# Kernel optimization log

Hardware: AMD Instinct MI355X
Metric: run time of the kernel (lower is better)

The kernel has to match this reference:

```python
import jax, jax.numpy as jnp
import numpy as np

N = 20000      # nodes per type
E = 320000     # edges per relation
F = 512        # raw feature dim
H = 4          # attention heads
C = 128        # hidden_channels per head
B = 64         # batch_size (num graphs)
HH = H * C
INNER = 64
NEG_SLOPE = 0.2


def _gatv2(x_src, x_dst, ei, Wl, Wr, att, b):
    """PyG GATv2Conv (concat=True, add_self_loops=True, neg_slope=0.2).
    x_src:[Ns,Fin] x_dst:[Nd,Fin'] ei:[2,E] Wl,Wr:[Fin,H*C] att:[H,C] b:[H*C].
    Returns [Nd, H*C]. Self-loop edges appended (inputs assumed loop-free)."""
    n_dst = x_dst.shape[0]
    loop = jnp.arange(min(x_src.shape[0], n_dst), dtype=ei.dtype)
    src = jnp.concatenate([ei[0], loop])
    dst = jnp.concatenate([ei[1], loop])
    xl = (x_src @ Wl).reshape(-1, H, C)   # source-side transform
    xr = (x_dst @ Wr).reshape(-1, H, C)   # target-side transform
    e = jax.nn.leaky_relu(xl[src] + xr[dst], NEG_SLOPE)   # [E',H,C]
    logit = jnp.einsum('ehc,hc->eh', e, att)               # [E',H]
    m = jax.ops.segment_max(logit, dst, num_segments=n_dst)
    m = jnp.where(jnp.isfinite(m), m, 0.0)
    p = jnp.exp(logit - m[dst])
    s = jax.ops.segment_sum(p, dst, num_segments=n_dst)
    alpha = p / jnp.maximum(s[dst], 1e-16)                 # per-dst softmax
    out = jax.ops.segment_sum(alpha[:, :, None] * xl[src], dst, num_segments=n_dst)
    return out.reshape(n_dst, HH) + b


def _layer(x_i, x_j, ei_ii, ei_jj, ei_ij, ei_ji, Wl, Wr, att, b):
    # relation order: 0:(x_i->x_i) 1:(x_j->x_j) 2:(x_i->x_j) 3:(x_j->x_i); HeteroConv aggr='sum'
    oi = _gatv2(x_i, x_i, ei_ii, Wl[0], Wr[0], att[0], b[0]) \
       + _gatv2(x_j, x_i, ei_ji, Wl[3], Wr[3], att[3], b[3])
    oj = _gatv2(x_j, x_j, ei_jj, Wl[1], Wr[1], att[1], b[1]) \
       + _gatv2(x_i, x_j, ei_ij, Wl[2], Wr[2], att[2], b[2])
    # head-sum + tanh: x.view(-1, heads, hidden).sum(1).tanh()
    oi = jnp.tanh(oi.reshape(-1, H, C).sum(axis=1))
    oj = jnp.tanh(oj.reshape(-1, H, C).sum(axis=1))
    return oi, oj


def setup_inputs() -> dict:
    key = jax.random.key(0)
    ks = jax.random.split(key, 24)
    inp = {
        'x_i': jax.random.normal(ks[0], (N, F), jnp.float32),
        'x_j': jax.random.normal(ks[1], (N, F), jnp.float32),
        'ei_ii': jax.random.randint(ks[2], (2, E), 0, N, jnp.int32),
        'ei_jj': jax.random.randint(ks[3], (2, E), 0, N, jnp.int32),
        'ei_ij': jax.random.randint(ks[4], (2, E), 0, N, jnp.int32),
        'ei_ji': jax.random.randint(ks[5], (2, E), 0, N, jnp.int32),
        'batch_i': jnp.sort(jax.random.randint(ks[6], (N,), 0, B, jnp.int32)),
        'batch_j': jnp.sort(jax.random.randint(ks[7], (N,), 0, B, jnp.int32)),
        'Wl0': jax.random.normal(ks[8], (4, F, HH), jnp.float32) / np.sqrt(F),
        'Wr0': jax.random.normal(ks[9], (4, F, HH), jnp.float32) / np.sqrt(F),
        'att0': jax.random.normal(ks[10], (4, H, C), jnp.float32) / np.sqrt(C),
        'b0': jnp.zeros((4, HH), jnp.float32),
        'Wl1': jax.random.normal(ks[11], (4, C, HH), jnp.float32) / np.sqrt(C),
        'Wr1': jax.random.normal(ks[12], (4, C, HH), jnp.float32) / np.sqrt(C),
        'att1': jax.random.normal(ks[13], (4, H, C), jnp.float32) / np.sqrt(C),
        'b1': jnp.zeros((4, HH), jnp.float32),
        'W_out': jax.random.normal(ks[14], (C, 1), jnp.float32) / np.sqrt(C),
        'b_out': jnp.zeros((1,), jnp.float32),
        'W_i': jax.random.normal(ks[15], (C, INNER), jnp.float32) / np.sqrt(C),
        'b_i': jnp.zeros((INNER,), jnp.float32),
        'W_j': jax.random.normal(ks[16], (C, INNER), jnp.float32) / np.sqrt(C),
        'b_j': jnp.zeros((INNER,), jnp.float32),
    }
    return inp


def reference(x_i, x_j, ei_ii, ei_jj, ei_ij, ei_ji, batch_i, batch_j,
              Wl0, Wr0, att0, b0, Wl1, Wr1, att1, b1,
              W_out, b_out, W_i, b_i, W_j, b_j):
    x_i, x_j = _layer(x_i, x_j, ei_ii, ei_jj, ei_ij, ei_ji, Wl0, Wr0, att0, b0)
    x_i, x_j = _layer(x_i, x_j, ei_ii, ei_jj, ei_ij, ei_ji, Wl1, Wr1, att1, b1)
    # global_add_pool per graph, then unsqueeze(1) + tanh
    p_i = jnp.tanh(jax.ops.segment_sum(x_i, batch_i, num_segments=B))[:, None, :]  # [B,1,C]
    p_j = jnp.tanh(jax.ops.segment_sum(x_j, batch_j, num_segments=B))[:, None, :]
    y_i = p_i @ W_i + b_i   # [B,1,INNER]
    y_j = p_j @ W_j + b_j
    x = (p_i + p_j)[:, 0, :]            # cat along dim=1 then sum(dim=1)
    logits = jax.nn.sigmoid(x @ W_out + b_out)   # [B,1]
    return (logits, y_i, y_j)
```

## Files before the change

### kernel.cpp

```cpp
#include <hip/hip_runtime.h>

#define NN      20000
#define EE      320000
#define ETOT    340000
#define FD      512
#define HH_     4
#define CD      128
#define HHD     512
#define BG      64
#define INNERD  64

typedef __attribute__((ext_vector_type(8))) short bf16x8;
typedef __attribute__((ext_vector_type(4))) float f32x4;

__device__ __forceinline__ float bf2f(unsigned v) { return __uint_as_float(v << 16); }
__device__ __forceinline__ unsigned short f2bf(float f) {
    unsigned u = __float_as_uint(f);
    unsigned r = 0x7fffu + ((u >> 16) & 1u);
    return (unsigned short)((u + r) >> 16);
}
__device__ __forceinline__ void load8bf(const unsigned short* p, float* f) {
    uint4 u = *reinterpret_cast<const uint4*>(p);
    f[0] = bf2f(u.x & 0xffffu); f[1] = bf2f(u.x >> 16);
    f[2] = bf2f(u.y & 0xffffu); f[3] = bf2f(u.y >> 16);
    f[4] = bf2f(u.z & 0xffffu); f[5] = bf2f(u.z >> 16);
    f[6] = bf2f(u.w & 0xffffu); f[7] = bf2f(u.w >> 16);
}
__device__ __forceinline__ void split_f32(float x, unsigned short& hi, unsigned short& lo) {
    unsigned u = __float_as_uint(x);
    hi = (unsigned short)(u >> 16);
    float r = x - bf2f(hi);
    lo = (unsigned short)(__float_as_uint(r) >> 16);
}
template <typename TA>
__device__ __forceinline__ void splitA(const TA* p, size_t i, unsigned short& hi, unsigned short& lo);
template <>
__device__ __forceinline__ void splitA<float>(const float* p, size_t i, unsigned short& hi, unsigned short& lo) {
    split_f32(p[i], hi, lo);
}
template <>
__device__ __forceinline__ void splitA<unsigned short>(const unsigned short* p, size_t i, unsigned short& hi, unsigned short& lo) {
    hi = p[i]; lo = 0;
}

__global__ __launch_bounds__(256) void csr_hist(const int* __restrict__ ei, int* __restrict__ cnt) {
    int e = blockIdx.x * blockDim.x + threadIdx.x;
    if (e < EE) atomicAdd(&cnt[ei[EE + e]], 1);
}

__global__ __launch_bounds__(1024) void csr_scan(const int* __restrict__ cnt,
                                                 int* __restrict__ rowptr,
                                                 int* __restrict__ cursor) {
    __shared__ int part[1024];
    int t = threadIdx.x;
    int base = t * 20;
    int s = 0;
    #pragma unroll
    for (int i = 0; i < 20; ++i) { int n = base + i; if (n < NN) s += cnt[n] + 1; }
    part[t] = s;
    __syncthreads();
    for (int off = 1; off < 1024; off <<= 1) {
        int v = (t >= off) ? part[t - off] : 0;
        __syncthreads();
        part[t] += v;
        __syncthreads();
    }
    int run = (t > 0) ? part[t - 1] : 0;
    #pragma unroll
    for (int i = 0; i < 20; ++i) {
        int n = base + i;
        if (n < NN) { rowptr[n] = run; cursor[n] = run; run += cnt[n] + 1; }
    }
    if (t == 1023) rowptr[NN] = run;
}

__global__ __launch_bounds__(256) void csr_scatter16(const int* __restrict__ ei,
                                                     int* __restrict__ cursor,
                                                     unsigned short* __restrict__ srcs) {
    int idx = blockIdx.x * blockDim.x + threadIdx.x;
    if (idx >= ETOT) return;
    int src, dst;
    if (idx < EE) { src = ei[idx]; dst = ei[EE + idx]; }
    else          { src = dst = idx - EE; }
    int pos = atomicAdd(&cursor[dst], 1);
    srcs[pos] = (unsigned short)src;
}

__global__ __launch_bounds__(256) void wsplit_t(const float* __restrict__ W,
                                                unsigned short* __restrict__ Whi,
                                                unsigned short* __restrict__ Wlo,
                                                int K)
{
    __shared__ float tile[64][65];
    const int nt = 512 / 64;
    const int kt = K / 64;
    int bid = blockIdx.x;
    int in = bid % nt; int ik = (bid / nt) % kt; int r = bid / (nt * kt);
    int t = threadIdx.x;
    const float* Wr_ = W + (size_t)r * K * 512;
    #pragma unroll
    for (int rep = 0; rep < 16; ++rep) {
        int idx = rep * 256 + t;
        int kk = idx >> 6, nn = idx & 63;
        tile[kk][nn] = Wr_[(size_t)(ik * 64 + kk) * 512 + in * 64 + nn];
    }
    __syncthreads();
    #pragma unroll
    for (int rep = 0; rep < 16; ++rep) {
        int idx = rep * 256 + t;
        int nn = idx >> 6, kk = idx & 63;
        unsigned short h, l; split_f32(tile[kk][nn], h, l);
        int n = in * 64 + nn;
        int k = ik * 64 + kk;
        size_t o = (size_t)r * 512 * K + ((size_t)(k >> 5) * 512 + n) * 32 + (k & 31);
        Whi[o] = h; Wlo[o] = l;
    }
}

template <typename TA, bool A_EXACT>
__device__ __forceinline__ void gemm_body(
    const TA* __restrict__ A, const unsigned short* __restrict__ Bhg,
    const unsigned short* __restrict__ Blg, unsigned short* __restrict__ C,
    int bx, int by, int M, int K, int N)
{
    __shared__ unsigned short Ah[128][40];
    __shared__ unsigned short Al[A_EXACT ? 1 : 128][40];

    const int tid = threadIdx.x;
    const int wave = tid >> 6, lane = tid & 63;
    const int quad = lane >> 4, lrow = lane & 15;
    const int wr = (wave >> 1) * 64, wc = (wave & 1) * 64;
    const int tileM = by * 128, tileN = bx * 128;

    const int srow = tid >> 1;
    const int sks  = (tid & 1) * 16;
    const int sgm  = tileM + srow;

    const size_t bfrag = ((size_t)(tileN + wc + lrow) << 5) + quad * 8;
    const size_t kblk  = (size_t)N << 5;

    f32x4 acc[4][4] = {};

    for (int k0 = 0; k0 < K; k0 += 32) {
        if constexpr (!A_EXACT) {
            bf16x8 ph[2] = {{}, {}}, pl[2] = {{}, {}};
            if (sgm < M) {
                const float* Ap = (const float*)A + (size_t)sgm * K + k0 + sks;
                #pragma unroll
                for (int s = 0; s < 2; ++s) {
                    float4 f0 = reinterpret_cast<const float4*>(Ap)[2 * s];
                    float4 f1 = reinterpret_cast<const float4*>(Ap)[2 * s + 1];
                    float xv[8] = {f0.x, f0.y, f0.z, f0.w, f1.x, f1.y, f1.z, f1.w};
                    #pragma unroll
                    for (int pp = 0; pp < 4; ++pp) {
                        unsigned u0 = __float_as_uint(xv[2 * pp]);
                        unsigned u1 = __float_as_uint(xv[2 * pp + 1]);
                        reinterpret_cast<unsigned*>(&ph[s])[pp] =
                            __builtin_amdgcn_perm(u1, u0, 0x07060302u);
                        float r0 = xv[2 * pp]     - __uint_as_float(u0 & 0xffff0000u);
                        float r1 = xv[2 * pp + 1] - __uint_as_float(u1 & 0xffff0000u);
                        reinterpret_cast<unsigned*>(&pl[s])[pp] =
                            __builtin_amdgcn_perm(__float_as_uint(r1), __float_as_uint(r0), 0x07060302u);
                    }
                }
            }
            *reinterpret_cast<bf16x8*>(&Ah[srow][sks])     = ph[0];
            *reinterpret_cast<bf16x8*>(&Ah[srow][sks + 8]) = ph[1];
            *reinterpret_cast<bf16x8*>(&Al[srow][sks])     = pl[0];
            *reinterpret_cast<bf16x8*>(&Al[srow][sks + 8]) = pl[1];
        } else {
            bf16x8 v0 = {}, v1 = {};
            if (sgm < M) {
                const unsigned short* Ap = (const unsigned short*)A + (size_t)sgm * K + k0 + sks;
                v0 = reinterpret_cast<const bf16x8*>(Ap)[0];
                v1 = reinterpret_cast<const bf16x8*>(Ap)[1];
            }
            *reinterpret_cast<bf16x8*>(&Ah[srow][sks])     = v0;
            *reinterpret_cast<bf16x8*>(&Ah[srow][sks + 8]) = v1;
        }
        bf16x8 bh[4], bl[4];
        {
            const unsigned short* Bb = Bhg + (size_t)(k0 >> 5) * kblk + bfrag;
            const unsigned short* Bc = Blg + (size_t)(k0 >> 5) * kblk + bfrag;
            #pragma unroll
            for (int ni = 0; ni < 4; ++ni) {
                bh[ni] = *reinterpret_cast<const bf16x8*>(Bb + ((size_t)ni << 9));
                bl[ni] = *reinterpret_cast<const bf16x8*>(Bc + ((size_t)ni << 9));
            }
        }
        __syncthreads();
        bf16x8 ah[4], al[4];
        #pragma unroll
        for (int mi = 0; mi < 4; ++mi) {
            ah[mi] = *reinterpret_cast<const bf16x8*>(&Ah[wr + mi * 16 + lrow][quad * 8]);
            if constexpr (!A_EXACT)
                al[mi] = *reinterpret_cast<const bf16x8*>(&Al[wr + mi * 16 + lrow][quad * 8]);
        }
        #pragma unroll
        for (int mi = 0; mi < 4; ++mi)
            #pragma unroll
            for (int ni = 0; ni < 4; ++ni) {
                acc[mi][ni] = __builtin_amdgcn_mfma_f32_16x16x32_bf16(
                    ah[mi], bh[ni], acc[mi][ni], 0, 0, 0);
                acc[mi][ni] = __builtin_amdgcn_mfma_f32_16x16x32_bf16(
                    ah[mi], bl[ni], acc[mi][ni], 0, 0, 0);
                if constexpr (!A_EXACT)
                    acc[mi][ni] = __builtin_amdgcn_mfma_f32_16x16x32_bf16(
                        al[mi], bh[ni], acc[mi][ni], 0, 0, 0);
            }
        __syncthreads();
    }
    #pragma unroll
    for (int mi = 0; mi < 4; ++mi) {
        #pragma unroll
        for (int ni = 0; ni < 4; ++ni) {
            int gcol = tileN + wc + ni * 16 + lrow;
            #pragma unroll
            for (int r = 0; r < 4; ++r) {
                int grow = tileM + wr + mi * 16 + quad * 4 + r;
                if (grow < M)
                    C[(size_t)grow * N + gcol] = f2bf(acc[mi][ni][r]);
            }
        }
    }
}

template <typename TA, bool A_EXACT>
__global__ __launch_bounds__(256, 3) void gemm_mfma_t(
    const TA* __restrict__ A0, const TA* __restrict__ A1,
    const unsigned short* __restrict__ B0h, const unsigned short* __restrict__ B0l,
    const unsigned short* __restrict__ B1h, const unsigned short* __restrict__ B1l,
    unsigned short* __restrict__ C0, unsigned short* __restrict__ C1,
    int M, int K, int N)
{
    const int gx = gridDim.x, gy = gridDim.y;
    const int nwg = gx * gy * (int)gridDim.z;
    int b = ((int)blockIdx.z * gy + blockIdx.y) * gx + blockIdx.x;
    int xcd = b & 7, q8 = nwg >> 3, r8 = nwg & 7;
    int work = (xcd < r8 ? xcd * (q8 + 1) : r8 * (q8 + 1) + (xcd - r8) * q8) + (b >> 3);
    int bx = work % gx; int t2 = work / gx; int by = t2 % gy; int bz = t2 / gy;

    const TA* A = bz ? A1 : A0;
    const unsigned short* Bhg = bz ? B1h : B0h;
    const unsigned short* Blg = bz ? B1l : B0l;
    unsigned short* C = bz ? C1 : C0;
    gemm_body<TA, A_EXACT>(A, Bhg, Blg, C, bx, by, M, K, N);
}

template <typename TA, bool A_EXACT>
__global__ __launch_bounds__(256, 3) void gemm_mfma_t4(
    const TA* __restrict__ A0, const TA* __restrict__ A1,
    const TA* __restrict__ A2, const TA* __restrict__ A3,
    const unsigned short* __restrict__ B0h, const unsigned short* __restrict__ B0l,
    const unsigned short* __restrict__ B1h, const unsigned short* __restrict__ B1l,
    const unsigned short* __restrict__ B2h, const unsigned short* __restrict__ B2l,
    const unsigned short* __restrict__ B3h, const unsigned short* __restrict__ B3l,
    unsigned short* __restrict__ C0, unsigned short* __restrict__ C1,
    unsigned short* __restrict__ C2, unsigned short* __restrict__ C3,
    int M, int K, int N)
{
    const int gx = gridDim.x, gy = gridDim.y;
    const int nwg = gx * gy * (int)gridDim.z;
    int b = ((int)blockIdx.z * gy + blockIdx.y) * gx + blockIdx.x;
    int xcd = b & 7, q8 = nwg >> 3, r8 = nwg & 7;
    int work = (xcd < r8 ? xcd * (q8 + 1) : r8 * (q8 + 1) + (xcd - r8) * q8) + (b >> 3);
    int bx = work % gx; int t2 = work / gx; int by = t2 % gy; int bz = t2 / gy;

    const TA* A = bz == 0 ? A0 : bz == 1 ? A1 : bz == 2 ? A2 : A3;
    const unsigned short* Bhg = bz == 0 ? B0h : bz == 1 ? B1h : bz == 2 ? B2h : B3h;
    const unsigned short* Blg = bz == 0 ? B0l : bz == 1 ? B1l : bz == 2 ? B2l : B3l;
    unsigned short* C = bz == 0 ? C0 : bz == 1 ? C1 : bz == 2 ? C2 : C3;
    gemm_body<TA, A_EXACT>(A, Bhg, Blg, C, bx, by, M, K, N);
}

template <typename TA, bool A_EXACT>
__global__ __launch_bounds__(256) void gemm_mfma(
    const TA* __restrict__ A0, const TA* __restrict__ A1,
    const float* __restrict__ B0, const float* __restrict__ B1, int ldb,
    unsigned short* __restrict__ C0, unsigned short* __restrict__ C1,
    int M, int K, int N)
{
    const TA* A = blockIdx.z ? A1 : A0;
    const float* B = blockIdx.z ? B1 : B0;
    unsigned short* C = blockIdx.z ? C1 : C0;

    __shared__ unsigned short Ah[64][40];
    __shared__ unsigned short Al[64][40];
    __shared__ unsigned short Bh[64][40];
    __shared__ unsigned short Bl[64][40];
    const int tid = threadIdx.x;
    const int wave = tid >> 6, lane = tid & 63;
    const int quad = lane >> 4, lrow = lane & 15;
    const int tileM = blockIdx.y * 64, tileN = blockIdx.x * 64;
    const int wm = (wave >> 1) * 32, wn = (wave & 1) * 32;

    f32x4 acc[2][2] = {};

    const int am = tid >> 2;
    const int aks = (tid & 3) * 8;
    const int bn = tid & 63;
    const int bk0 = (tid >> 6) * 8;

    for (int k0 = 0; k0 < K; k0 += 32) {
        {
            int gm = tileM + am;
            bf16x8 ph = {}, pl = {};
            if (gm < M) {
                #pragma unroll
                for (int j = 0; j < 8; ++j) {
                    unsigned short h, l;
                    splitA(A, (size_t)gm * K + k0 + aks + j, h, l);
                    ph[j] = (short)h; pl[j] = (short)l;
                }
            }
            *reinterpret_cast<bf16x8*>(&Ah[am][aks]) = ph;
            if (!A_EXACT) *reinterpret_cast<bf16x8*>(&Al[am][aks]) = pl;
        }
        {
            bf16x8 ph, pl;
            #pragma unroll
            for (int j = 0; j < 8; ++j) {
                unsigned short h, l;
                split_f32(B[(size_t)(k0 + bk0 + j) * ldb + tileN + bn], h, l);
                ph[j] = (short)h; pl[j] = (short)l;
            }
            *reinterpret_cast<bf16x8*>(&Bh[bn][bk0]) = ph;
            *reinterpret_cast<bf16x8*>(&Bl[bn][bk0]) = pl;
        }
        __syncthreads();
        bf16x8 ah[2], al[2], bh[2], bl[2];
        #pragma unroll
        for (int mi = 0; mi < 2; ++mi) {
            ah[mi] = *reinterpret_cast<const bf16x8*>(&Ah[wm + mi * 16 + lrow][quad * 8]);
            if (!A_EXACT)
                al[mi] = *reinterpret_cast<const bf16x8*>(&Al[wm + mi * 16 + lrow][quad * 8]);
        }
        #pragma unroll
        for (int ni = 0; ni < 2; ++ni) {
            bh[ni] = *reinterpret_cast<const bf16x8*>(&Bh[wn + ni * 16 + lrow][quad * 8]);
            bl[ni] = *reinterpret_cast<const bf16x8*>(&Bl[wn + ni * 16 + lrow][quad * 8]);
        }
        #pragma unroll
        for (int mi = 0; mi < 2; ++mi)
            #pragma unroll
            for (int ni = 0; ni < 2; ++ni) {
                acc[mi][ni] = __builtin_amdgcn_mfma_f32_16x16x32_bf16(
                    ah[mi], bh[ni], acc[mi][ni], 0, 0, 0);
                acc[mi][ni] = __builtin_amdgcn_mfma_f32_16x16x32_bf16(
                    ah[mi], bl[ni], acc[mi][ni], 0, 0, 0);
                if (!A_EXACT)
                    acc[mi][ni] = __builtin_amdgcn_mfma_f32_16x16x32_bf16(
                        al[mi], bh[ni], acc[mi][ni], 0, 0, 0);
            }
        __syncthreads();
    }
    #pragma unroll
    for (int mi = 0; mi < 2; ++mi) {
        #pragma unroll
        for (int ni = 0; ni < 2; ++ni) {
            int gcol = tileN + wn + ni * 16 + lrow;
            #pragma unroll
            for (int r = 0; r < 4; ++r) {
                int grow = tileM + wm + mi * 16 + quad * 4 + r;
                if (grow < M)
                    C[(size_t)grow * N + gcol] = f2bf(acc[mi][ni][r]);
            }
        }
    }
}

__global__ __launch_bounds__(256) void fused_aggr1(
    const int* __restrict__ rowptr, const unsigned short* __restrict__ srcs,
    const unsigned short* __restrict__ xl, const unsigned short* __restrict__ xr,
    const float* __restrict__ att,
    float* __restrict__ acc, int add_in, int fin_mode,
    const float* __restrict__ bA, const float* __restrict__ bB,
    unsigned short* __restrict__ z,
    const int* __restrict__ batch, float* __restrict__ pool)
{
    int dst = (int)((blockIdx.x * (size_t)blockDim.x + threadIdx.x) >> 6);
    int lane = threadIdx.x & 63;
    if (dst >= NN) return;
    int beg = rowptr[dst], end = rowptr[dst + 1];

    unsigned ub = *reinterpret_cast<const unsigned*>(xr + (size_t)dst * CD + lane * 2);
    float br0 = bf2f(ub & 0xffffu), br1 = bf2f(ub >> 16);
    float ta0 = att[lane * 2], ta1 = att[lane * 2 + 1];

    float n0 = 0.f, n1 = 0.f, den = 0.f;
    for (int k = beg; k < end; ++k) {
        int src = srcs[k];
        unsigned ua = *reinterpret_cast<const unsigned*>(xl + (size_t)src * CD + lane * 2);
        float a0 = bf2f(ua & 0xffffu), a1 = bf2f(ua >> 16);
        float v0 = a0 + br0, v1 = a1 + br1;
        v0 = (v0 > 0.f) ? v0 : 0.2f * v0;
        v1 = (v1 > 0.f) ? v1 : 0.2f * v1;
        float d = v0 * ta0 + v1 * ta1;
        #pragma unroll
        for (int off = 1; off < 64; off <<= 1)
            d += __shfl_xor(d, off);
        float p = expf(d);
        n0 += p * a0; n1 += p * a1; den += p;
    }
    float o0 = n0 / den, o1 = n1 / den;
    size_t ai = (size_t)dst * CD + lane * 2;
    if (add_in) { o0 += acc[ai]; o1 += acc[ai + 1]; }
    if (fin_mode == 0) {
        acc[ai] = o0; acc[ai + 1] = o1;
    } else {
        int c0 = lane * 2;
        float bb0 = 0.f, bb1 = 0.f;
        #pragma unroll
        for (int h = 0; h < HH_; ++h) {
            bb0 += bA[h * CD + c0]     + bB[h * CD + c0];
            bb1 += bA[h * CD + c0 + 1] + bB[h * CD + c0 + 1];
        }
        o0 = tanhf(o0 + bb0);
        o1 = tanhf(o1 + bb1);
        if (fin_mode == 1) {
            z[ai] = f2bf(o0); z[ai + 1] = f2bf(o1);
        } else {
            int b = batch[dst];
            atomicAdd(&pool[(size_t)b * CD + c0],     o0);
            atomicAdd(&pool[(size_t)b * CD + c0 + 1], o1);
        }
    }
}

__device__ __forceinline__ void gat_rel(
    const int* __restrict__ rp, const unsigned short* __restrict__ sr,
    const unsigned short* __restrict__ xl, const unsigned short* __restrict__ xr,
    const float* __restrict__ att, int dst, int lane, float* o)
{
    int beg = rp[dst], end = rp[dst + 1];
    float br[8], ta[8];
    load8bf(xr + (size_t)dst * HHD + lane * 8, br);
    #pragma unroll
    for (int j = 0; j < 8; ++j) ta[j] = att[lane * 8 + j];

    float n[8] = {}; float den = 0.f;
    int k = beg;
    for (; k + 2 <= end; k += 2) {
        int s0 = sr[k], s1 = sr[k + 1];
        float a0[8], a1[8];
        load8bf(xl + (size_t)s0 * HHD + lane * 8, a0);
        load8bf(xl + (size_t)s1 * HHD + lane * 8, a1);
        float d0 = 0.f, d1 = 0.f;
        #pragma unroll
        for (int j = 0; j < 8; ++j) {
            float v0 = a0[j] + br[j];
            v0 = fmaxf(v0, 0.2f * v0);
            d0 += v0 * ta[j];
            float v1 = a1[j] + br[j];
            v1 = fmaxf(v1, 0.2f * v1);
            d1 += v1 * ta[j];
        }
        d0 += __shfl_xor(d0, 1);  d1 += __shfl_xor(d1, 1);
        d0 += __shfl_xor(d0, 2);  d1 += __shfl_xor(d1, 2);
        d0 += __shfl_xor(d0, 4);  d1 += __shfl_xor(d1, 4);
        d0 += __shfl_xor(d0, 8);  d1 += __shfl_xor(d1, 8);
        float p0 = __expf(d0), p1 = __expf(d1);
        den += p0;
        #pragma unroll
        for (int j = 0; j < 8; ++j) n[j] += p0 * a0[j];
        den += p1;
        #pragma unroll
        for (int j = 0; j < 8; ++j) n[j] += p1 * a1[j];
    }
    if (k < end) {
        int s0 = sr[k];
        float a0[8];
        load8bf(xl + (size_t)s0 * HHD + lane * 8, a0);
        float d0 = 0.f;
        #pragma unroll
        for (int j = 0; j < 8; ++j) {
            float v0 = a0[j] + br[j];
            v0 = fmaxf(v0, 0.2f * v0);
            d0 += v0 * ta[j];
        }
        d0 += __shfl_xor(d0, 1);
        d0 += __shfl_xor(d0, 2);
        d0 += __shfl_xor(d0, 4);
        d0 += __shfl_xor(d0, 8);
        float p0 = __expf(d0);
        den += p0;
        #pragma unroll
        for (int j = 0; j < 8; ++j) n[j] += p0 * a0[j];
    }
    float inv = 1.f / den;
    #pragma unroll
    for (int j = 0; j < 8; ++j) {
        o[j] = n[j] * inv;
        o[j] += __shfl_xor(o[j], 16);
        o[j] += __shfl_xor(o[j], 32);
    }
}

__global__ __launch_bounds__(256) void fused_aggr4(
    const int* __restrict__ rowptr, const unsigned short* __restrict__ srcs,
    const unsigned short* __restrict__ xl, const unsigned short* __restrict__ xr,
    const float* __restrict__ att,
    float* __restrict__ acc, int add_in, int fin_mode,
    const float* __restrict__ bA, const float* __restrict__ bB,
    unsigned short* __restrict__ z,
    const int* __restrict__ batch, float* __restrict__ pool)
{
    int dst = (int)((blockIdx.x * (size_t)blockDim.x + threadIdx.x) >> 6);
    int lane = threadIdx.x & 63;
    if (dst >= NN) return;

    float o[8];
    gat_rel(rowptr, srcs, xl, xr, att, dst, lane, o);

    if (lane < 16) {
        size_t ai = (size_t)dst * CD + lane * 8;
        if (add_in) {
            #pragma unroll
            for (int j = 0; j < 8; ++j) o[j] += acc[ai + j];
        }
        if (fin_mode == 0) {
            #pragma unroll
            for (int j = 0; j < 8; ++j) acc[ai + j] = o[j];
        } else {
            int c0 = lane * 8;
            #pragma unroll
            for (int j = 0; j < 8; ++j) {
                float bb = 0.f;
                #pragma unroll
                for (int h = 0; h < HH_; ++h)
                    bb += bA[h * CD + c0 + j] + bB[h * CD + c0 + j];
                o[j] = tanhf(o[j] + bb);
            }
            if (fin_mode == 1) {
                #pragma unroll
                for (int j = 0; j < 8; ++j) z[ai + j] = f2bf(o[j]);
            } else {
                #pragma unroll
                for (int j = 0; j < 8; ++j) acc[ai + j] = o[j];
            }
        }
    }
}

__global__ __launch_bounds__(256) void fused_aggr4d(
    const int* __restrict__ rp0, const unsigned short* __restrict__ sr0,
    const unsigned short* __restrict__ xl0, const unsigned short* __restrict__ xr0,
    const float* __restrict__ attA,
    const int* __restrict__ rp1, const unsigned short* __restrict__ sr1,
    const unsigned short* __restrict__ xl1, const unsigned short* __restrict__ xr1,
    const float* __restrict__ attB,
    float* __restrict__ acc, int fin_mode,
    const float* __restrict__ bA, const float* __restrict__ bB,
    unsigned short* __restrict__ z,
    const int* __restrict__ batch, float* __restrict__ pool)
{
    int dst = (int)((blockIdx.x * (size_t)blockDim.x + threadIdx.x) >> 6);
    int lane = threadIdx.x & 63;
    if (dst >= NN) return;

    float o0[8], o1[8];
    gat_rel(rp0, sr0, xl0, xr0, attA, dst, lane, o0);
    gat_rel(rp1, sr1, xl1, xr1, attB, dst, lane, o1);
    #pragma unroll
    for (int j = 0; j < 8; ++j) o1[j] += o0[j];

    if (lane < 16) {
        size_t ai = (size_t)dst * CD + lane * 8;
        int c0 = lane * 8;
        #pragma unroll
        for (int j = 0; j < 8; ++j) {
            float bb = 0.f;
            #pragma unroll
            for (int h = 0; h < HH_; ++h)
                bb += bA[h * CD + c0 + j] + bB[h * CD + c0 + j];
            o1[j] = tanhf(o1[j] + bb);
        }
        if (fin_mode == 1) {
            #pragma unroll
            for (int j = 0; j < 8; ++j) z[ai + j] = f2bf(o1[j]);
        } else {
            #pragma unroll
            for (int j = 0; j < 8; ++j) acc[ai + j] = o1[j];
        }
    }
}

__global__ __launch_bounds__(512) void pool_reduce(
    const float* __restrict__ acc, const int* __restrict__ batch,
    float* __restrict__ pool)
{
    int b = blockIdx.x;
    int t = threadIdx.x & (CD - 1);
    int q = threadIdx.x >> 7;
    int lo, hi;
    { int l = 0, r = NN; while (l < r) { int m = (l + r) >> 1; if (batch[m] < b) l = m + 1; else r = m; } lo = l; }
    { int l = lo, r = NN; while (l < r) { int m = (l + r) >> 1; if (batch[m] <= b) l = m + 1; else r = m; } hi = l; }
    float s = 0.f;
    for (int nrow = lo + q; nrow < hi; nrow += 4)
        s += acc[(size_t)nrow * CD + t];
    __shared__ float red[4][CD];
    red[q][t] = s;
    __syncthreads();
    if (q == 0)
        pool[(size_t)b * CD + t] = red[0][t] + red[1][t] + red[2][t] + red[3][t];
}

__global__ __launch_bounds__(128) void head_kernel(
    const float* __restrict__ pool_i, const float* __restrict__ pool_j,
    const float* __restrict__ W_out, const float* __restrict__ b_out,
    const float* __restrict__ W_i, const float* __restrict__ b_i,
    const float* __restrict__ W_j, const float* __restrict__ b_j,
    float* __restrict__ out)
{
    int b = blockIdx.x;
    int t = threadIdx.x;
    __shared__ float pi[CD], pj[CD];
    pi[t] = tanhf(pool_i[(size_t)b * CD + t]);
    pj[t] = tanhf(pool_j[(size_t)b * CD + t]);
    __syncthreads();
    if (t < INNERD) {
        float a = b_i[t];
        for (int c = 0; c < CD; ++c) a += pi[c] * W_i[c * INNERD + t];
        out[BG + (size_t)b * INNERD + t] = a;
    } else {
        int k = t - INNERD;
        float a = b_j[k];
        for (int c = 0; c < CD; ++c) a += pj[c] * W_j[c * INNERD + k];
        out[BG + BG * INNERD + (size_t)b * INNERD + k] = a;
    }
    if (t == 0) {
        float a = b_out[0];
        for (int c = 0; c < CD; ++c) a += (pi[c] + pj[c]) * W_out[c];
        out[b] = 1.f / (1.f + expf(-a));
    }
}

struct Ws {
    unsigned short *xl, *xr, *xl2, *xr2, *z_i, *z_j;
    float* acc;
    int *rowptr[4];
    unsigned short *srcs[4];
    int *cnt, *cursor;
    float *pool_i, *pool_j;
    unsigned short *wt0l_h, *wt0l_l, *wt0r_h, *wt0r_l;
    unsigned short *wt1l_h, *wt1l_l, *wt1r_h, *wt1r_l;
};

static void build_csr(const int* ei, int* rowptr, unsigned short* srcs,
                      int* cnt, int* cursor, hipStream_t stream) {
    hipMemsetAsync(cnt, 0, NN * sizeof(int), stream);
    csr_hist<<<(EE + 255) / 256, 256, 0, stream>>>(ei, cnt);
    csr_scan<<<1, 1024, 0, stream>>>(cnt, rowptr, cursor);
    csr_scatter16<<<(ETOT + 255) / 256, 256, 0, stream>>>(ei, cursor, srcs);
}

template <typename TA, bool A_EXACT>
static void run_group_fat_m(const TA* srcA[2], const TA* dstA[2],
                            const int* rp[2], const unsigned short* sr[2],
                            const int rids[2], int K,
                            const unsigned short* WTl_h, const unsigned short* WTl_l,
                            const unsigned short* WTr_h, const unsigned short* WTr_l,
                            const float* att, const float* bias, int fin_mode,
                            unsigned short* zout, const int* batch, float* pool,
                            const Ws& w, hipStream_t stream)
{
    dim3 gg(HHD / 128, (NN + 127) / 128, 4);
    size_t off0 = (size_t)rids[0] * HHD * K;
    size_t off1 = (size_t)rids[1] * HHD * K;
    gemm_mfma_t4<TA, A_EXACT><<<gg, 256, 0, stream>>>(
        srcA[0], dstA[0], srcA[1], dstA[1],
        WTl_h + off0, WTl_l + off0, WTr_h + off0, WTr_l + off0,
        WTl_h + off1, WTl_l + off1, WTr_h + off1, WTr_l + off1,
        w.xl, w.xr, w.xl2, w.xr2, NN, K, HHD);
    fused_aggr4d<<<NN / 4, 256, 0, stream>>>(
        rp[0], sr[0], w.xl, w.xr, att + (size_t)rids[0] * HHD,
        rp[1], sr[1], w.xl2, w.xr2, att + (size_t)rids[1] * HHD,
        w.acc, fin_mode,
        bias + (size_t)rids[0] * HHD, bias + (size_t)rids[1] * HHD,
        zout, batch, pool);
}

template <typename TA, bool A_EXACT>
static void run_group_fat_t(const TA* srcA[2], const TA* dstA[2],
                            const int* rp[2], const unsigned short* sr[2],
                            const int rids[2], int K,
                            const unsigned short* WTl_h, const unsigned short* WTl_l,
                            const unsigned short* WTr_h, const unsigned short* WTr_l,
                            const float* att, const float* bias, int fin_mode,
                            unsigned short* zout, const int* batch, float* pool,
                            const Ws& w, hipStream_t stream)
{
    dim3 gg(HHD / 128, (NN + 127) / 128, 2);
    const int ablocks = NN / 4;
    for (int q = 0; q < 2; ++q) {
        int r = rids[q];
        size_t off = (size_t)r * HHD * K;
        gemm_mfma_t<TA, A_EXACT><<<gg, 256, 0, stream>>>(
            srcA[q], dstA[q],
            WTl_h + off, WTl_l + off, WTr_h + off, WTr_l + off,
            w.xl, w.xr, NN, K, HHD);
        int fm = (q == 1) ? fin_mode : 0;
        fused_aggr4<<<ablocks, 256, 0, stream>>>(
            rp[q], sr[q], w.xl, w.xr,
            att + (size_t)r * HHD,
            w.acc, q > 0 ? 1 : 0, fm,
            bias + (size_t)rids[0] * HHD, bias + (size_t)rids[1] * HHD,
            zout, batch, pool);
    }
}

template <typename TA, bool A_EXACT>
static void run_group_fat(const TA* srcA[2], const TA* dstA[2],
                          const int* rp[2], const unsigned short* sr[2],
                          const int rids[2], int K,
                          const float* Wl, const float* Wr, const float* att,
                          const float* bias, int fin_mode,
                          unsigned short* zout, const int* batch, float* pool,
                          const Ws& w, hipStream_t stream)
{
    dim3 gg(HHD / 64, (NN + 63) / 64, 2);
    const int ablocks = NN / 4;
    for (int q = 0; q < 2; ++q) {
        int r = rids[q];
        gemm_mfma<TA, A_EXACT><<<gg, 256, 0, stream>>>(
            srcA[q], dstA[q],
            Wl + (size_t)r * K * HHD, Wr + (size_t)r * K * HHD, HHD,
            w.xl, w.xr, NN, K, HHD);
        int fm = (q == 1) ? fin_mode : 0;
        fused_aggr4<<<ablocks, 256, 0, stream>>>(
            rp[q], sr[q], w.xl, w.xr,
            att + (size_t)r * HHD,
            w.acc, q > 0 ? 1 : 0, fm,
            bias + (size_t)rids[0] * HHD, bias + (size_t)rids[1] * HHD,
            zout, batch, pool);
    }
}

template <typename TA, bool A_EXACT>
static void run_group_thin(const TA* srcA[2], const TA* dstA[2],
                           const int* eis[2], const int rids[2], int K,
                           const float* Wl, const float* Wr, const float* att,
                           const float* bias, int fin_mode,
                           unsigned short* zout, const int* batch, float* pool,
                           const Ws& w, hipStream_t stream)
{
    dim3 gg(2, (NN + 63) / 64, 2);
    const int ablocks = NN / 4;
    for (int q = 0; q < 2; ++q) {
        int r = rids[q];
        build_csr(eis[q], w.rowptr[0], w.srcs[0], w.cnt, w.cursor, stream);
        for (int h = 0; h < HH_; ++h) {
            const float* WlS = Wl + (size_t)r * K * HHD + h * CD;
            const float* WrS = Wr + (size_t)r * K * HHD + h * CD;
            gemm_mfma<TA, A_EXACT><<<gg, 256, 0, stream>>>(
                srcA[q], dstA[q], WlS, WrS, HHD, w.xl, w.xr, NN, K, CD);
            int pass = q * HH_ + h;
            int fm = (pass == 2 * HH_ - 1) ? fin_mode : 0;
            fused_aggr1<<<ablocks, 256, 0, stream>>>(
                w.rowptr[0], w.srcs[0], w.xl, w.xr,
                att + (size_t)r * HHD + h * CD,
                w.acc, pass > 0 ? 1 : 0, fm,
                bias + (size_t)rids[0] * HHD, bias + (size_t)rids[1] * HHD,
                zout, batch, pool);
        }
    }
}

extern "C" void kernel_launch(void* const* d_in, const int* in_sizes, int n_in,
                              void* d_out, int out_size, void* d_ws, size_t ws_size,
                              hipStream_t stream)
{
    const float* x_i   = (const float*)d_in[0];
    const float* x_j   = (const float*)d_in[1];
    const int* ei_ii   = (const int*)d_in[2];
    const int* ei_jj   = (const int*)d_in[3];
    const int* ei_ij   = (const int*)d_in[4];
    const int* ei_ji   = (const int*)d_in[5];
    const int* batch_i = (const int*)d_in[6];
    const int* batch_j = (const int*)d_in[7];
    const float* Wl0   = (const float*)d_in[8];
    const float* Wr0   = (const float*)d_in[9];
    const float* att0  = (const float*)d_in[10];
    const float* b0    = (const float*)d_in[11];
    const float* Wl1   = (const float*)d_in[12];
    const float* Wr1   = (const float*)d_in[13];
    const float* att1  = (const float*)d_in[14];
    const float* b1    = (const float*)d_in[15];
    const float* W_out = (const float*)d_in[16];
    const float* b_out = (const float*)d_in[17];
    const float* W_i   = (const float*)d_in[18];
    const float* b_i   = (const float*)d_in[19];
    const float* W_j   = (const float*)d_in[20];
    const float* b_j   = (const float*)d_in[21];
    float* out = (float*)d_out;

    const size_t FAT2_BYTES = (size_t)NN * HHD * 2 * 2 + (size_t)NN * CD * 4
                            + (size_t)NN * CD * 2 * 2 + 4 * (size_t)ETOT * 2
                            + 4 * (size_t)(NN + 4) * 4 + (size_t)NN * 4 * 2
                            + (size_t)BG * CD * 4 * 2;
    const size_t FAT1_BYTES = (size_t)NN * HHD * 2 * 2 + (size_t)NN * CD * 4
                            + (size_t)NN * CD * 2 * 2 + (size_t)ETOT * 2
                            + (size_t)(NN + 4) * 4 + (size_t)NN * 4 * 2
                            + (size_t)BG * CD * 4 * 2;
    const size_t WT0_ONE = (size_t)4 * 512 * 512 * 2;
    const size_t WT1_ONE = (size_t)4 * 512 * 128 * 2;
    const size_t WT_BYTES = 4 * WT0_ONE + 4 * WT1_ONE;
    const size_t X2_BYTES = 2 * (size_t)NN * HHD * 2;

    const int ncsr = (ws_size >= FAT2_BYTES) ? 4 : 1;
    const bool fat = (ws_size >= FAT1_BYTES);
    const bool fat_t = (ws_size >= FAT2_BYTES + WT_BYTES);
    const bool fat_m = (ws_size >= FAT2_BYTES + WT_BYTES + X2_BYTES);

    Ws w;
    char* p = (char*)d_ws;
    size_t xbytes = fat ? (size_t)NN * HHD * 2 : (size_t)NN * CD * 2;
    w.xl     = (unsigned short*)p; p += xbytes;
    w.xr     = (unsigned short*)p; p += xbytes;
    w.acc    = (float*)p;          p += (size_t)NN * CD * 4;
    w.z_i    = (unsigned short*)p; p += (size_t)NN * CD * 2;
    w.z_j    = (unsigned short*)p; p += (size_t)NN * CD * 2;
    for (int r = 0; r < 4; ++r) {
        int rr = (r < ncsr) ? r : 0;
        if (r < ncsr) {
            w.rowptr[r] = (int*)p;            p += (size_t)(NN + 4) * 4;
            w.srcs[r]   = (unsigned short*)p; p += (size_t)ETOT * 2;
        } else {
            w.rowptr[r] = w.rowptr[rr]; w.srcs[r] = w.srcs[rr];
        }
    }
    w.cnt    = (int*)p;            p += (size_t)NN * 4;
    w.cursor = (int*)p;            p += (size_t)NN * 4;
    w.pool_i = (float*)p;          p += (size_t)BG * CD * 4;
    w.pool_j = (float*)p;          p += (size_t)BG * CD * 4;
    if (fat_t) {
        w.wt0l_h = (unsigned short*)p; p += WT0_ONE;
        w.wt0l_l = (unsigned short*)p; p += WT0_ONE;
        w.wt0r_h = (unsigned short*)p; p += WT0_ONE;
        w.wt0r_l = (unsigned short*)p; p += WT0_ONE;
        w.wt1l_h = (unsigned short*)p; p += WT1_ONE;
        w.wt1l_l = (unsigned short*)p; p += WT1_ONE;
        w.wt1r_h = (unsigned short*)p; p += WT1_ONE;
        w.wt1r_l = (unsigned short*)p; p += WT1_ONE;
    }
    if (fat_m) {
        w.xl2 = (unsigned short*)p; p += (size_t)NN * HHD * 2;
        w.xr2 = (unsigned short*)p; p += (size_t)NN * HHD * 2;
    }

    hipMemsetAsync(w.pool_i, 0, (size_t)BG * CD * sizeof(float), stream);
    hipMemsetAsync(w.pool_j, 0, (size_t)BG * CD * sizeof(float), stream);

    const int* eis_all[4] = { ei_ii, ei_jj, ei_ij, ei_ji };
    const float* srcA0_i[2] = { x_i, x_j };  const float* dstA0_i[2] = { x_i, x_i };
    const float* srcA0_j[2] = { x_j, x_i };  const float* dstA0_j[2] = { x_j, x_j };
    const int rids_i[2] = { 0, 3 };
    const int rids_j[2] = { 1, 2 };
    const unsigned short* srcA1_i[2] = { w.z_i, w.z_j };
    const unsigned short* dstA1_i[2] = { w.z_i, w.z_i };
    const unsigned short* srcA1_j[2] = { w.z_j, w.z_i };
    const unsigned short* dstA1_j[2] = { w.z_j, w.z_j };

    if (fat_t) {
        for (int r = 0; r < 4; ++r)
            build_csr(eis_all[r], w.rowptr[r], w.srcs[r], w.cnt, w.cursor, stream);
        wsplit_t<<<4 * (FD / 64) * 8, 256, 0, stream>>>(Wl0, w.wt0l_h, w.wt0l_l, FD);
        wsplit_t<<<4 * (FD / 64) * 8, 256, 0, stream>>>(Wr0, w.wt0r_h, w.wt0r_l, FD);
        wsplit_t<<<4 * (CD / 64) * 8, 256, 0, stream>>>(Wl1, w.wt1l_h, w.wt1l_l, CD);
        wsplit_t<<<4 * (CD / 64) * 8, 256, 0, stream>>>(Wr1, w.wt1r_h, w.wt1r_l, CD);

        const int* rp_i[2] = { w.rowptr[0], w.rowptr[3] };
        const unsigned short* sr_i[2] = { w.srcs[0], w.srcs[3] };
        const int* rp_j[2] = { w.rowptr[1], w.rowptr[2] };
        const unsigned short* sr_j[2] = { w.srcs[1], w.srcs[2] };

        if (fat_m) {
            run_group_fat_m<float, false>(srcA0_i, dstA0_i, rp_i, sr_i, rids_i, FD,
                                          w.wt0l_h, w.wt0l_l, w.wt0r_h, w.wt0r_l,
                                          att0, b0, 1, w.z_i, nullptr, nullptr, w, stream);
            run_group_fat_m<float, false>(srcA0_j, dstA0_j, rp_j, sr_j, rids_j, FD,
                                          w.wt0l_h, w.wt0l_l, w.wt0r_h, w.wt0r_l,
                                          att0, b0, 1, w.z_j, nullptr, nullptr, w, stream);
            run_group_fat_m<unsigned short, true>(srcA1_i, dstA1_i, rp_i, sr_i, rids_i, CD,
                                                  w.wt1l_h, w.wt1l_l, w.wt1r_h, w.wt1r_l,
                                                  att1, b1, 2, nullptr, batch_i, w.pool_i, w, stream);
            pool_reduce<<<BG, 512, 0, stream>>>(w.acc, batch_i, w.pool_i);
            run_group_fat_m<unsigned short, true>(srcA1_j, dstA1_j, rp_j, sr_j, rids_j, CD,
                                                  w.wt1l_h, w.wt1l_l, w.wt1r_h, w.wt1r_l,
                                                  att1, b1, 2, nullptr, batch_j, w.pool_j, w, stream);
            pool_reduce<<<BG, 512, 0, stream>>>(w.acc, batch_j, w.pool_j);
        } else {
            run_group_fat_t<float, false>(srcA0_i, dstA0_i, rp_i, sr_i, rids_i, FD,
                                          w.wt0l_h, w.wt0l_l, w.wt0r_h, w.wt0r_l,
                                          att0, b0, 1, w.z_i, nullptr, nullptr, w, stream);
            run_group_fat_t<float, false>(srcA0_j, dstA0_j, rp_j, sr_j, rids_j, FD,
                                          w.wt0l_h, w.wt0l_l, w.wt0r_h, w.wt0r_l,
                                          att0, b0, 1, w.z_j, nullptr, nullptr, w, stream);
            run_group_fat_t<unsigned short, true>(srcA1_i, dstA1_i, rp_i, sr_i, rids_i, CD,
                                                  w.wt1l_h, w.wt1l_l, w.wt1r_h, w.wt1r_l,
                                                  att1, b1, 2, nullptr, batch_i, w.pool_i, w, stream);
            pool_reduce<<<BG, 512, 0, stream>>>(w.acc, batch_i, w.pool_i);
            run_group_fat_t<unsigned short, true>(srcA1_j, dstA1_j, rp_j, sr_j, rids_j, CD,
                                                  w.wt1l_h, w.wt1l_l, w.wt1r_h, w.wt1r_l,
                                                  att1, b1, 2, nullptr, batch_j, w.pool_j, w, stream);
            pool_reduce<<<BG, 512, 0, stream>>>(w.acc, batch_j, w.pool_j);
        }
    } else if (fat) {
        if (ncsr == 4) {
            for (int r = 0; r < 4; ++r)
                build_csr(eis_all[r], w.rowptr[r], w.srcs[r], w.cnt, w.cursor, stream);
            const int* rp_i[2] = { w.rowptr[0], w.rowptr[3] };
            const unsigned short* sr_i[2] = { w.srcs[0], w.srcs[3] };
            const int* rp_j[2] = { w.rowptr[1], w.rowptr[2] };
            const unsigned short* sr_j[2] = { w.srcs[1], w.srcs[2] };
            run_group_fat<float, false>(srcA0_i, dstA0_i, rp_i, sr_i, rids_i, FD,
                                        Wl0, Wr0, att0, b0, 1, w.z_i, nullptr, nullptr, w, stream);
            run_group_fat<float, false>(srcA0_j, dstA0_j, rp_j, sr_j, rids_j, FD,
                                        Wl0, Wr0, att0, b0, 1, w.z_j, nullptr, nullptr, w, stream);
            run_group_fat<unsigned short, true>(srcA1_i, dstA1_i, rp_i, sr_i, rids_i, CD,
                                                Wl1, Wr1, att1, b1, 2, nullptr, batch_i, w.pool_i, w, stream);
            pool_reduce<<<BG, 512, 0, stream>>>(w.acc, batch_i, w.pool_i);
            run_group_fat<unsigned short, true>(srcA1_j, dstA1_j, rp_j, sr_j, rids_j, CD,
                                                Wl1, Wr1, att1, b1, 2, nullptr, batch_j, w.pool_j, w, stream);
            pool_reduce<<<BG, 512, 0, stream>>>(w.acc, batch_j, w.pool_j);
        } else {
            for (int pass = 0; pass < 4; ++pass) {
                const int* rids = (pass & 1) ? rids_j : rids_i;
                for (int q = 0; q < 2; ++q) {
                    int r = rids[q];
                    build_csr(eis_all[r], w.rowptr[0], w.srcs[0], w.cnt, w.cursor, stream);
                    dim3 gg(HHD / 64, (NN + 63) / 64, 2);
                    if (pass < 2) {
                        const float* sa = (pass == 0) ? srcA0_i[q] : srcA0_j[q];
                        const float* da = (pass == 0) ? dstA0_i[q] : dstA0_j[q];
                        gemm_mfma<float, false><<<gg, 256, 0, stream>>>(
                            sa, da, Wl0 + (size_t)r * FD * HHD, Wr0 + (size_t)r * FD * HHD,
                            HHD, w.xl, w.xr, NN, FD, HHD);
                        fused_aggr4<<<NN / 4, 256, 0, stream>>>(
                            w.rowptr[0], w.srcs[0], w.xl, w.xr, att0 + (size_t)r * HHD,
                            w.acc, q, (q == 1) ? 1 : 0,
                            b0 + (size_t)rids[0] * HHD, b0 + (size_t)rids[1] * HHD,
                            (pass == 0) ? w.z_i : w.z_j, nullptr, nullptr);
                    } else {
                        const unsigned short* sa = (pass == 2) ? srcA1_i[q] : srcA1_j[q];
                        const unsigned short* da = (pass == 2) ? dstA1_i[q] : dstA1_j[q];
                        gemm_mfma<unsigned short, true><<<gg, 256, 0, stream>>>(
                            sa, da, Wl1 + (size_t)r * CD * HHD, Wr1 + (size_t)r * CD * HHD,
                            HHD, w.xl, w.xr, NN, CD, HHD);
                        fused_aggr4<<<NN / 4, 256, 0, stream>>>(
                            w.rowptr[0], w.srcs[0], w.xl, w.xr, att1 + (size_t)r * HHD,
                            w.acc, q, (q == 1) ? 2 : 0,
                            b1 + (size_t)rids[0] * HHD, b1 + (size_t)rids[1] * HHD,
                            nullptr, (pass == 2) ? batch_i : batch_j,
                            (pass == 2) ? w.pool_i : w.pool_j);
                    }
                }
                if (pass == 2)
                    pool_reduce<<<BG, 512, 0, stream>>>(w.acc, batch_i, w.pool_i);
                else if (pass == 3)
                    pool_reduce<<<BG, 512, 0, stream>>>(w.acc, batch_j, w.pool_j);
            }
        }
    } else {
        const int* eis_i[2] = { ei_ii, ei_ji };
        const int* eis_j[2] = { ei_jj, ei_ij };
        run_group_thin<float, false>(srcA0_i, dstA0_i, eis_i, rids_i, FD, Wl0, Wr0, att0, b0,
                                     1, w.z_i, nullptr, nullptr, w, stream);
        run_group_thin<float, false>(srcA0_j, dstA0_j, eis_j, rids_j, FD, Wl0, Wr0, att0, b0,
                                     1, w.z_j, nullptr, nullptr, w, stream);
        run_group_thin<unsigned short, true>(srcA1_i, dstA1_i, eis_i, rids_i, CD, Wl1, Wr1, att1, b1,
                                             2, nullptr, batch_i, w.pool_i, w, stream);
        run_group_thin<unsigned short, true>(srcA1_j, dstA1_j, eis_j, rids_j, CD, Wl1, Wr1, att1, b1,
                                             2, nullptr, batch_j, w.pool_j, w, stream);
    }

    head_kernel<<<BG, 128, 0, stream>>>(w.pool_i, w.pool_j, W_out, b_out,
                                        W_i, b_i, W_j, b_j, out);
}
```

Before: 1.414 ms.

## Batch CSR build across relations and interleave dual-relation edge aggregation

The four per-relation CSR builds are merged into single histogram, scan and scatter launches over all relations. The cnt and cursor workspace arrays grow to hold all four relations, and rowptr and srcs become contiguous. In the dual-relation aggregation kernel, edges of both relations are now processed in one interleaved loop, four gathers at a time, with tail loops draining the remainder. The goal is fewer launches and more memory-level parallelism in the gather-bound loop, at the cost of higher register pressure.

Result: faster. 1.352 ms (-4.4%).

```diff
diff --git a/kernel.cpp b/kernel.cpp
--- a/kernel.cpp
+++ b/kernel.cpp
@@ -84,6 +84,65 @@
     else          { src = dst = idx - EE; }
     int pos = atomicAdd(&cursor[dst], 1);
     srcs[pos] = (unsigned short)src;
+}
+
+__global__ __launch_bounds__(256) void csr_hist4(
+    const int* __restrict__ e0, const int* __restrict__ e1,
+    const int* __restrict__ e2, const int* __restrict__ e3,
+    int* __restrict__ cnt)
+{
+    int idx = blockIdx.x * blockDim.x + threadIdx.x;
+    if (idx >= 4 * EE) return;
+    int r = idx / EE, e = idx - r * EE;
+    const int* ei = r == 0 ? e0 : r == 1 ? e1 : r == 2 ? e2 : e3;
+    atomicAdd(&cnt[r * NN + ei[EE + e]], 1);
+}
+
+__global__ __launch_bounds__(1024) void csr_scan4(const int* __restrict__ cnt_all,
+                                                  int* __restrict__ rowptr_all,
+                                                  int* __restrict__ cursor_all)
+{
+    const int r = blockIdx.x;
+    const int* cnt = cnt_all + r * NN;
+    int* rowptr = rowptr_all + r * (NN + 4);
+    int* cursor = cursor_all + r * NN;
+    __shared__ int part[1024];
+    int t = threadIdx.x;
+    int base = t * 20;
+    int s = 0;
+    #pragma unroll
+    for (int i = 0; i < 20; ++i) { int n = base + i; if (n < NN) s += cnt[n] + 1; }
+    part[t] = s;
+    __syncthreads();
+    for (int off = 1; off < 1024; off <<= 1) {
+        int v = (t >= off) ? part[t - off] : 0;
+        __syncthreads();
+        part[t] += v;
+        __syncthreads();
+    }
+    int run = (t > 0) ? part[t - 1] : 0;
+    #pragma unroll
+    for (int i = 0; i < 20; ++i) {
+        int n = base + i;
+        if (n < NN) { rowptr[n] = run; cursor[n] = run; run += cnt[n] + 1; }
+    }
+    if (t == 1023) rowptr[NN] = run;
+}
+
+__global__ __launch_bounds__(256) void csr_scatter4(
+    const int* __restrict__ e0, const int* __restrict__ e1,
+    const int* __restrict__ e2, const int* __restrict__ e3,
+    int* __restrict__ cursor_all, unsigned short* __restrict__ srcs_all)
+{
+    int idx = blockIdx.x * blockDim.x + threadIdx.x;
+    if (idx >= 4 * ETOT) return;
+    int r = idx / ETOT, t = idx - r * ETOT;
+    const int* ei = r == 0 ? e0 : r == 1 ? e1 : r == 2 ? e2 : e3;
+    int src, dst;
+    if (t < EE) { src = ei[t]; dst = ei[EE + t]; }
+    else        { src = dst = t - EE; }
+    int pos = atomicAdd(&cursor_all[r * NN + dst], 1);
+    srcs_all[(size_t)r * ETOT + pos] = (unsigned short)src;
 }
 
 __global__ __launch_bounds__(256) void wsplit_t(const float* __restrict__ W,
@@ -427,6 +486,54 @@
     }
 }
 
+__device__ __forceinline__ float edge_logit(const float* a, const float* br, const float* ta) {
+    float d = 0.f;
+    #pragma unroll
+    for (int j = 0; j < 8; ++j) {
+        float v = a[j] + br[j];
+        v = fmaxf(v, 0.2f * v);
+        d += v * ta[j];
+    }
+    return d;
+}
+__device__ __forceinline__ float quad_reduce(float d) {
+    d += __shfl_xor(d, 1);
+    d += __shfl_xor(d, 2);
+    d += __shfl_xor(d, 4);
+    d += __shfl_xor(d, 8);
+    return d;
+}
+__device__ __forceinline__ void gat_drain(
+    const unsigned short* __restrict__ sr, const unsigned short* __restrict__ xl,
+    const float* br, const float* ta, int k, int e, float* n, float& den, int lane)
+{
+    for (; k + 2 <= e; k += 2) {
+        int s0 = sr[k], s1 = sr[k + 1];
+        float A0[8], A1[8];
+        load8bf(xl + (size_t)s0 * HHD + lane * 8, A0);
+        load8bf(xl + (size_t)s1 * HHD + lane * 8, A1);
+        float d0 = quad_reduce(edge_logit(A0, br, ta));
+        float d1 = quad_reduce(edge_logit(A1, br, ta));
+        float p0 = __expf(d0), p1 = __expf(d1);
+        den += p0;
+        #pragma unroll
+        for (int j = 0; j < 8; ++j) n[j] += p0 * A0[j];
+        den += p1;
+        #pragma unroll
+        for (int j = 0; j < 8; ++j) n[j] += p1 * A1[j];
+    }
+    if (k < e) {
+        int s0 = sr[k];
+        float A0[8];
+        load8bf(xl + (size_t)s0 * HHD + lane * 8, A0);
+        float d0 = quad_reduce(edge_logit(A0, br, ta));
+        float p0 = __expf(d0);
+        den += p0;
+        #pragma unroll
+        for (int j = 0; j < 8; ++j) n[j] += p0 * A0[j];
+    }
+}
+
 __device__ __forceinline__ void gat_rel(
     const int* __restrict__ rp, const unsigned short* __restrict__ sr,
     const unsigned short* __restrict__ xl, const unsigned short* __restrict__ xr,
@@ -437,62 +544,77 @@
     load8bf(xr + (size_t)dst * HHD + lane * 8, br);
     #pragma unroll
     for (int j = 0; j < 8; ++j) ta[j] = att[lane * 8 + j];
-
     float n[8] = {}; float den = 0.f;
-    int k = beg;
-    for (; k + 2 <= end; k += 2) {
-        int s0 = sr[k], s1 = sr[k + 1];
-        float a0[8], a1[8];
-        load8bf(xl + (size_t)s0 * HHD + lane * 8, a0);
-        load8bf(xl + (size_t)s1 * HHD + lane * 8, a1);
-        float d0 = 0.f, d1 = 0.f;
-        #pragma unroll
-        for (int j = 0; j < 8; ++j) {
-            float v0 = a0[j] + br[j];
-            v0 = fmaxf(v0, 0.2f * v0);
-            d0 += v0 * ta[j];
-            float v1 = a1[j] + br[j];
-            v1 = fmaxf(v1, 0.2f * v1);
-            d1 += v1 * ta[j];
-        }
-        d0 += __shfl_xor(d0, 1);  d1 += __shfl_xor(d1, 1);
-        d0 += __shfl_xor(d0, 2);  d1 += __shfl_xor(d1, 2);
-        d0 += __shfl_xor(d0, 4);  d1 += __shfl_xor(d1, 4);
-        d0 += __shfl_xor(d0, 8);  d1 += __shfl_xor(d1, 8);
-        float p0 = __expf(d0), p1 = __expf(d1);
-        den += p0;
-        #pragma unroll
-        for (int j = 0; j < 8; ++j) n[j] += p0 * a0[j];
-        den += p1;
-        #pragma unroll
-        for (int j = 0; j < 8; ++j) n[j] += p1 * a1[j];
-    }
-    if (k < end) {
-        int s0 = sr[k];
-        float a0[8];
-        load8bf(xl + (size_t)s0 * HHD + lane * 8, a0);
-        float d0 = 0.f;
-        #pragma unroll
-        for (int j = 0; j < 8; ++j) {
-            float v0 = a0[j] + br[j];
-            v0 = fmaxf(v0, 0.2f * v0);
-            d0 += v0 * ta[j];
-        }
-        d0 += __shfl_xor(d0, 1);
-        d0 += __shfl_xor(d0, 2);
-        d0 += __shfl_xor(d0, 4);
-        d0 += __shfl_xor(d0, 8);
-        float p0 = __expf(d0);
-        den += p0;
-        #pragma unroll
-        for (int j = 0; j < 8; ++j) n[j] += p0 * a0[j];
-    }
+    gat_drain(sr, xl, br, ta, beg, end, n, den, lane);
     float inv = 1.f / den;
     #pragma unroll
     for (int j = 0; j < 8; ++j) {
         o[j] = n[j] * inv;
         o[j] += __shfl_xor(o[j], 16);
         o[j] += __shfl_xor(o[j], 32);
+    }
+}
+
+__device__ __forceinline__ void gat_rel2(
+    const int* __restrict__ rp0, const unsigned short* __restrict__ sr0,
+    const unsigned short* __restrict__ xl0, const unsigned short* __restrict__ xr0,
+    const float* __restrict__ attA,
+    const int* __restrict__ rp1, const unsigned short* __restrict__ sr1,
+    const unsigned short* __restrict__ xl1, const unsigned short* __restrict__ xr1,
+    const float* __restrict__ attB,
+    int dst, int lane, float* o0, float* o1)
+{
+    int k0 = rp0[dst], e0 = rp0[dst + 1];
+    int k1 = rp1[dst], e1 = rp1[dst + 1];
+    float br0[8], br1[8], ta0[8], ta1[8];
+    load8bf(xr0 + (size_t)dst * HHD + lane * 8, br0);
+    load8bf(xr1 + (size_t)dst * HHD + lane * 8, br1);
+    #pragma unroll
+    for (int j = 0; j < 8; ++j) { ta0[j] = attA[lane * 8 + j]; ta1[j] = attB[lane * 8 + j]; }
+
+    float n0[8] = {}, n1[8] = {};
+    float den0 = 0.f, den1 = 0.f;
+
+    while (k0 + 2 <= e0 && k1 + 2 <= e1) {
+        int sa0 = sr0[k0], sa1 = sr0[k0 + 1];
+        int sb0 = sr1[k1], sb1 = sr1[k1 + 1];
+        float A0[8], A1[8], B0[8], B1[8];
+        load8bf(xl0 + (size_t)sa0 * HHD + lane * 8, A0);
+        load8bf(xl0 + (size_t)sa1 * HHD + lane * 8, A1);
+        load8bf(xl1 + (size_t)sb0 * HHD + lane * 8, B0);
+        load8bf(xl1 + (size_t)sb1 * HHD + lane * 8, B1);
+        float dA0 = quad_reduce(edge_logit(A0, br0, ta0));
+        float dA1 = quad_reduce(edge_logit(A1, br0, ta0));
+        float dB0 = quad_reduce(edge_logit(B0, br1, ta1));
+        float dB1 = quad_reduce(edge_logit(B1, br1, ta1));
+        float pA0 = __expf(dA0), pA1 = __expf(dA1);
+        float pB0 = __expf(dB0), pB1 = __expf(dB1);
+        den0 += pA0;
+        #pragma unroll
+        for (int j = 0; j < 8; ++j) n0[j] += pA0 * A0[j];
+        den0 += pA1;
+        #pragma unroll
+        for (int j = 0; j < 8; ++j) n0[j] += pA1 * A1[j];
+        den1 += pB0;
+        #pragma unroll
+        for (int j = 0; j < 8; ++j) n1[j] += pB0 * B0[j];
+        den1 += pB1;
+        #pragma unroll
+        for (int j = 0; j < 8; ++j) n1[j] += pB1 * B1[j];
+        k0 += 2; k1 += 2;
+    }
+    gat_drain(sr0, xl0, br0, ta0, k0, e0, n0, den0, lane);
+    gat_drain(sr1, xl1, br1, ta1, k1, e1, n1, den1, lane);
+
+    float i0 = 1.f / den0, i1 = 1.f / den1;
+    #pragma unroll
+    for (int j = 0; j < 8; ++j) {
+        o0[j] = n0[j] * i0;
+        o0[j] += __shfl_xor(o0[j], 16);
+        o0[j] += __shfl_xor(o0[j], 32);
+        o1[j] = n1[j] * i1;
+        o1[j] += __shfl_xor(o1[j], 16);
+        o1[j] += __shfl_xor(o1[j], 32);
     }
 }
 
@@ -559,8 +681,7 @@
     if (dst >= NN) return;
 
     float o0[8], o1[8];
-    gat_rel(rp0, sr0, xl0, xr0, attA, dst, lane, o0);
-    gat_rel(rp1, sr1, xl1, xr1, attB, dst, lane, o1);
+    gat_rel2(rp0, sr0, xl0, xr0, attA, rp1, sr1, xl1, xr1, attB, dst, lane, o0, o1);
     #pragma unroll
     for (int j = 0; j < 8; ++j) o1[j] += o0[j];
 
@@ -796,7 +917,7 @@
 
     const size_t FAT2_BYTES = (size_t)NN * HHD * 2 * 2 + (size_t)NN * CD * 4
                             + (size_t)NN * CD * 2 * 2 + 4 * (size_t)ETOT * 2
-                            + 4 * (size_t)(NN + 4) * 4 + (size_t)NN * 4 * 2
+                            + 4 * (size_t)(NN + 4) * 4 + 4 * (size_t)NN * 4 * 2
                             + (size_t)BG * CD * 4 * 2;
     const size_t FAT1_BYTES = (size_t)NN * HHD * 2 * 2 + (size_t)NN * CD * 4
                             + (size_t)NN * CD * 2 * 2 + (size_t)ETOT * 2
@@ -820,17 +941,17 @@
     w.acc    = (float*)p;          p += (size_t)NN * CD * 4;
     w.z_i    = (unsigned short*)p; p += (size_t)NN * CD * 2;
     w.z_j    = (unsigned short*)p; p += (size_t)NN * CD * 2;
-    for (int r = 0; r < 4; ++r) {
-        int rr = (r < ncsr) ? r : 0;
-        if (r < ncsr) {
-            w.rowptr[r] = (int*)p;            p += (size_t)(NN + 4) * 4;
-            w.srcs[r]   = (unsigned short*)p; p += (size_t)ETOT * 2;
-        } else {
-            w.rowptr[r] = w.rowptr[rr]; w.srcs[r] = w.srcs[rr];
-        }
-    }
-    w.cnt    = (int*)p;            p += (size_t)NN * 4;
-    w.cursor = (int*)p;            p += (size_t)NN * 4;
+    {
+        int* rowptr_all = (int*)p;            p += (size_t)ncsr * (NN + 4) * 4;
+        unsigned short* srcs_all = (unsigned short*)p; p += (size_t)ncsr * ETOT * 2;
+        for (int r = 0; r < 4; ++r) {
+            int rr = (r < ncsr) ? r : 0;
+            w.rowptr[r] = rowptr_all + (size_t)rr * (NN + 4);
+            w.srcs[r]   = srcs_all + (size_t)rr * ETOT;
+        }
+    }
+    w.cnt    = (int*)p;            p += (size_t)ncsr * NN * 4;
+    w.cursor = (int*)p;            p += (size_t)ncsr * NN * 4;
     w.pool_i = (float*)p;          p += (size_t)BG * CD * 4;
     w.pool_j = (float*)p;          p += (size_t)BG * CD * 4;
     if (fat_t) {
@@ -862,8 +983,12 @@
     const unsigned short* dstA1_j[2] = { w.z_j, w.z_j };
 
     if (fat_t) {
-        for (int r = 0; r < 4; ++r)
-            build_csr(eis_all[r], w.rowptr[r], w.srcs[r], w.cnt, w.cursor, stream);
+        hipMemsetAsync(w.cnt, 0, 4 * NN * sizeof(int), stream);
+        csr_hist4<<<(4 * EE + 255) / 256, 256, 0, stream>>>(
+            ei_ii, ei_jj, ei_ij, ei_ji, w.cnt);
+        csr_scan4<<<4, 1024, 0, stream>>>(w.cnt, w.rowptr[0], w.cursor);
+        csr_scatter4<<<(4 * ETOT + 255) / 256, 256, 0, stream>>>(
+            ei_ii, ei_jj, ei_ij, ei_ji, w.cursor, w.srcs[0]);
         wsplit_t<<<4 * (FD / 64) * 8, 256, 0, stream>>>(Wl0, w.wt0l_h, w.wt0l_l, FD);
         wsplit_t<<<4 * (FD / 64) * 8, 256, 0, stream>>>(Wr0, w.wt0r_h, w.wt0r_l, FD);
         wsplit_t<<<4 * (CD / 64) * 8, 256, 0, stream>>>(Wl1, w.wt1l_h, w.wt1l_l, CD);
```
